# Kernel optimization log

Measured on AMD Instinct MI355X. Metric: run time of the kernel, lower is better.

The kernel has to match this reference:

```python
import jax, jax.numpy as jnp
import numpy as np

DIM = 256
HEADS = 8
SR = 2
EPS = 1e-5


def setup_inputs() -> dict:
    key = jax.random.key(0)
    ks = jax.random.split(key, 8)
    B, N, C = 4, 4096, DIM
    s = 0.02
    return {
        "x": jax.random.normal(ks[0], (B, N, C), dtype=jnp.float32),
        "H": 64,
        "W": 64,
        # sequence-reduction conv (Conv2d dim->dim, k=SR, stride=SR), OIHW
        "sr_w": jax.random.normal(ks[1], (C, C, SR, SR), dtype=jnp.float32) * s,
        "sr_b": jnp.zeros((C,), dtype=jnp.float32),
        "ln_g": jnp.ones((C,), dtype=jnp.float32),
        "ln_b": jnp.zeros((C,), dtype=jnp.float32),
        # torch Linear weights: y = x @ W.T (qkv_bias=False)
        "q_w": jax.random.normal(ks[2], (C, C), dtype=jnp.float32) * s,
        "kv_w": jax.random.normal(ks[3], (2 * C, C), dtype=jnp.float32) * s,
        "proj_w": jax.random.normal(ks[4], (C, C), dtype=jnp.float32) * s,
        "proj_b": jnp.zeros((C,), dtype=jnp.float32),
    }


def reference(x, H, W, sr_w, sr_b, ln_g, ln_b, q_w, kv_w, proj_w, proj_b):
    B, N, C = x.shape
    h, d = HEADS, C // HEADS
    scale = d ** -0.5

    # q: [B, h, N, d]
    q = (x @ q_w.T).reshape(B, N, h, d).transpose(0, 2, 1, 3)

    # sequence reduction: [B,N,C] -> [B,C,H,W] -> conv(k=SR, s=SR) -> [B, N', C]
    x_ = x.transpose(0, 2, 1).reshape(B, C, H, W)
    x_ = jax.lax.conv_general_dilated(
        x_, sr_w, window_strides=(SR, SR), padding="VALID",
        dimension_numbers=("NCHW", "OIHW", "NCHW"))
    x_ = x_ + sr_b[None, :, None, None]
    x_ = x_.reshape(B, C, -1).transpose(0, 2, 1)  # [B, N', C]

    # LayerNorm over C
    mu = x_.mean(-1, keepdims=True)
    var = x_.var(-1, keepdims=True)
    x_ = (x_ - mu) * jax.lax.rsqrt(var + EPS) * ln_g + ln_b

    # kv: [2, B, h, N', d]
    kv = (x_ @ kv_w.T).reshape(B, -1, 2, h, d).transpose(2, 0, 3, 1, 4)
    k, v = kv[0], kv[1]

    attn = jnp.einsum("bhnd,bhmd->bhnm", q, k) * scale
    attn = jax.nn.softmax(attn, axis=-1)  # attn_drop = 0 -> identity
    out = jnp.einsum("bhnm,bhmd->bhnd", attn, v)
    out = out.transpose(0, 2, 1, 3).reshape(B, N, C)

    return out @ proj_w.T + proj_b  # proj_drop = 0 -> identity
```

## Files before the change

### kernel.cpp

```cpp
#include <hip/hip_runtime.h>
#include <hip/hip_bf16.h>


typedef __attribute__((ext_vector_type(8))) short bf16x8;
typedef __attribute__((ext_vector_type(8))) unsigned short u16x8;
typedef __attribute__((ext_vector_type(4))) float f32x4;
typedef __attribute__((ext_vector_type(16))) float f32x16;
typedef __attribute__((ext_vector_type(2))) unsigned u32x2v;
typedef __attribute__((ext_vector_type(4))) unsigned u32x4v;

__device__ inline unsigned short f2bf(float f) {
  unsigned u = __float_as_uint(f);
  u += 0x7fffu + ((u >> 16) & 1u);
  return (unsigned short)(u >> 16);
}

__global__ __launch_bounds__(256) void prep_kernel(
    const float* __restrict__ x, unsigned short* __restrict__ x_bf,
    const float* __restrict__ srw, unsigned short* __restrict__ srw_bf) {
  const int bid = blockIdx.x, t = threadIdx.x;
  if (bid < 2048) {
    int i = bid * 256 + t;
    float4 a = reinterpret_cast<const float4*>(x)[i * 2];
    float4 b = reinterpret_cast<const float4*>(x)[i * 2 + 1];
    ushort4 lo, hi;
    lo.x = f2bf(a.x); lo.y = f2bf(a.y); lo.z = f2bf(a.z); lo.w = f2bf(a.w);
    hi.x = f2bf(b.x); hi.y = f2bf(b.y); hi.z = f2bf(b.z); hi.w = f2bf(b.w);
    reinterpret_cast<ushort4*>(x_bf)[i * 2] = lo;
    reinterpret_cast<ushort4*>(x_bf)[i * 2 + 1] = hi;
  } else {
    int o = bid - 2048;
    float4 v = reinterpret_cast<const float4*>(srw + (size_t)o * 1024)[t];
    srw_bf[(size_t)o * 1024 + 0 * 256 + t] = f2bf(v.x);
    srw_bf[(size_t)o * 1024 + 1 * 256 + t] = f2bf(v.y);
    srw_bf[(size_t)o * 1024 + 2 * 256 + t] = f2bf(v.z);
    srw_bf[(size_t)o * 1024 + 3 * 256 + t] = f2bf(v.w);
  }
}

__device__ __forceinline__ void gemm_body_q(
    const unsigned short* __restrict__ A, const float* __restrict__ W,
    unsigned short* __restrict__ C, int K, int N, float oscale,
    int m0, int n0, unsigned short* Asb, unsigned short* Bsb) {
  const int tid = threadIdx.x;
  const int w = tid >> 6, l = tid & 63, c = l & 15, g = l >> 4;
  const int wr = w >> 1, wc = w & 1;
  const int ar = tid >> 1, ah = tid & 1;
  const int bn = tid >> 2, bq = tid & 3;

  f32x4 acc[4][2];
#pragma unroll
  for (int mt = 0; mt < 4; ++mt)
#pragma unroll
    for (int nt = 0; nt < 2; ++nt)
#pragma unroll
      for (int r = 0; r < 4; ++r) acc[mt][nt][r] = 0.f;

  for (int k0 = 0; k0 < K; k0 += 32) {
    __syncthreads();
    {
      const unsigned short* asrc = A + (size_t)(m0 + ar) * K + k0 + ah * 16;
      u16x8 a0 = *reinterpret_cast<const u16x8*>(asrc);
      u16x8 a1 = *reinterpret_cast<const u16x8*>(asrc + 8);
      *reinterpret_cast<u16x8*>(&Asb[ar * 40 + ah * 16]) = a0;
      *reinterpret_cast<u16x8*>(&Asb[ar * 40 + ah * 16 + 8]) = a1;
    }
    {
      const float* wsrc = W + (size_t)(n0 + bn) * K + k0 + bq * 8;
      float4 w0 = *reinterpret_cast<const float4*>(wsrc);
      float4 w1 = *reinterpret_cast<const float4*>(wsrc + 4);
      u16x8 wb;
      wb[0] = f2bf(w0.x); wb[1] = f2bf(w0.y); wb[2] = f2bf(w0.z); wb[3] = f2bf(w0.w);
      wb[4] = f2bf(w1.x); wb[5] = f2bf(w1.y); wb[6] = f2bf(w1.z); wb[7] = f2bf(w1.w);
      *reinterpret_cast<u16x8*>(&Bsb[bn * 40 + bq * 8]) = wb;
    }
    __syncthreads();
    bf16x8 af[4], bfr[2];
#pragma unroll
    for (int mt = 0; mt < 4; ++mt)
      af[mt] = *reinterpret_cast<const bf16x8*>(
          &Asb[(wr * 64 + mt * 16 + c) * 40 + g * 8]);
#pragma unroll
    for (int nt = 0; nt < 2; ++nt)
      bfr[nt] = *reinterpret_cast<const bf16x8*>(
          &Bsb[(wc * 32 + nt * 16 + c) * 40 + g * 8]);
#pragma unroll
    for (int mt = 0; mt < 4; ++mt)
#pragma unroll
      for (int nt = 0; nt < 2; ++nt)
        acc[mt][nt] = __builtin_amdgcn_mfma_f32_16x16x32_bf16(
            af[mt], bfr[nt], acc[mt][nt], 0, 0, 0);
  }

#pragma unroll
  for (int mt = 0; mt < 4; ++mt)
#pragma unroll
    for (int nt = 0; nt < 2; ++nt) {
      int row = m0 + wr * 64 + mt * 16 + g * 4;
      int col = n0 + wc * 32 + nt * 16 + c;
#pragma unroll
      for (int r = 0; r < 4; ++r)
        C[(size_t)(row + r) * N + col] = f2bf(acc[mt][nt][r] * oscale);
    }
}

__device__ __forceinline__ void conv_body(
    const unsigned short* __restrict__ Xb, const unsigned short* __restrict__ Wp,
    const float* __restrict__ bias, float* __restrict__ C,
    int m0, int n0, unsigned short* Asb, unsigned short* Bsb) {
  const int tid = threadIdx.x;
  const int w = tid >> 6, l = tid & 63, c = l & 15, g = l >> 4;
  const int wr = w >> 1, wc = w & 1;
  const int sr = tid >> 2, sh = tid & 3;

  int base[4];
  {
    int row = m0 + sr;
    int b = row >> 10, o = row & 1023, oh = o >> 5, ow = o & 31;
#pragma unroll
    for (int tap = 0; tap < 4; ++tap) {
      int n = ((oh << 1) + (tap >> 1)) * 64 + (ow << 1) + (tap & 1);
      base[tap] = ((b << 12) + n) << 8;
    }
  }

  f32x4 acc[2][2];
#pragma unroll
  for (int mt = 0; mt < 2; ++mt)
#pragma unroll
    for (int nt = 0; nt < 2; ++nt)
#pragma unroll
      for (int r = 0; r < 4; ++r) acc[mt][nt][r] = 0.f;

  for (int k0 = 0; k0 < 1024; k0 += 32) {
    const int tap = k0 >> 8, ci0 = (k0 & 255) + sh * 8;
    __syncthreads();
    u16x8 av = *reinterpret_cast<const u16x8*>(&Xb[base[tap] + ci0]);
    *reinterpret_cast<u16x8*>(&Asb[sr * 40 + sh * 8]) = av;
    u16x8 wv = *reinterpret_cast<const u16x8*>(
        &Wp[(size_t)(n0 + sr) * 1024 + k0 + sh * 8]);
    *reinterpret_cast<u16x8*>(&Bsb[sr * 40 + sh * 8]) = wv;
    __syncthreads();
    bf16x8 af[2], bfr[2];
#pragma unroll
    for (int mt = 0; mt < 2; ++mt)
      af[mt] = *reinterpret_cast<const bf16x8*>(
          &Asb[(wr * 32 + mt * 16 + c) * 40 + g * 8]);
#pragma unroll
    for (int nt = 0; nt < 2; ++nt)
      bfr[nt] = *reinterpret_cast<const bf16x8*>(
          &Bsb[(wc * 32 + nt * 16 + c) * 40 + g * 8]);
#pragma unroll
    for (int mt = 0; mt < 2; ++mt)
#pragma unroll
      for (int nt = 0; nt < 2; ++nt)
        acc[mt][nt] = __builtin_amdgcn_mfma_f32_16x16x32_bf16(
            af[mt], bfr[nt], acc[mt][nt], 0, 0, 0);
  }

#pragma unroll
  for (int mt = 0; mt < 2; ++mt)
#pragma unroll
    for (int nt = 0; nt < 2; ++nt) {
      int row = m0 + wr * 32 + mt * 16 + g * 4;
      int col = n0 + wc * 32 + nt * 16 + c;
      float bv = bias[col];
#pragma unroll
      for (int r = 0; r < 4; ++r)
        C[(size_t)(row + r) * 256 + col] = acc[mt][nt][r] + bv;
    }
}

__global__ __launch_bounds__(256) void qconv_kernel(
    const unsigned short* __restrict__ x_bf, const float* __restrict__ q_w,
    unsigned short* __restrict__ q_bf, const unsigned short* __restrict__ srw_bf,
    const float* __restrict__ sr_b, float* __restrict__ xred, float qscale) {
  __shared__ unsigned short smem[128 * 40 + 64 * 40];
  const int bid = blockIdx.x;
  if (bid < 512) {
    gemm_body_q(x_bf, q_w, q_bf, 256, 256, qscale,
                (bid >> 2) * 128, (bid & 3) * 64, smem, smem + 128 * 40);
  } else {
    int cb = bid - 512;
    conv_body(x_bf, srw_bf, sr_b, xred,
              (cb >> 2) * 64, (cb & 3) * 64, smem, smem + 64 * 40);
  }
}

template <bool BF16_OUT, bool HAS_BIAS, bool KV_MODE>
__global__ __launch_bounds__(256) void mfma_gemm(
    const unsigned short* __restrict__ A, const float* __restrict__ W,
    const float* __restrict__ bias, void* __restrict__ Cv,
    void* __restrict__ Vtp, int M, int N, int K, float oscale) {
  __shared__ unsigned short Asb[128 * 40];
  __shared__ unsigned short Bsb[64 * 40];
  const int tid = threadIdx.x;
  const int w = tid >> 6, l = tid & 63, c = l & 15, g = l >> 4;
  const int wr = w >> 1, wc = w & 1;
  const int m0 = blockIdx.y * 128, n0 = blockIdx.x * 64;
  const int ar = tid >> 1, ah = tid & 1;
  const int bn = tid >> 2, bq = tid & 3;

  f32x4 acc[4][2];
#pragma unroll
  for (int mt = 0; mt < 4; ++mt)
#pragma unroll
    for (int nt = 0; nt < 2; ++nt)
#pragma unroll
      for (int r = 0; r < 4; ++r) acc[mt][nt][r] = 0.f;

  for (int k0 = 0; k0 < K; k0 += 32) {
    __syncthreads();
    {
      const unsigned short* asrc = A + (size_t)(m0 + ar) * K + k0 + ah * 16;
      u16x8 a0 = *reinterpret_cast<const u16x8*>(asrc);
      u16x8 a1 = *reinterpret_cast<const u16x8*>(asrc + 8);
      *reinterpret_cast<u16x8*>(&Asb[ar * 40 + ah * 16]) = a0;
      *reinterpret_cast<u16x8*>(&Asb[ar * 40 + ah * 16 + 8]) = a1;
    }
    {
      const float* wsrc = W + (size_t)(n0 + bn) * K + k0 + bq * 8;
      float4 w0 = *reinterpret_cast<const float4*>(wsrc);
      float4 w1 = *reinterpret_cast<const float4*>(wsrc + 4);
      u16x8 wb;
      wb[0] = f2bf(w0.x); wb[1] = f2bf(w0.y); wb[2] = f2bf(w0.z); wb[3] = f2bf(w0.w);
      wb[4] = f2bf(w1.x); wb[5] = f2bf(w1.y); wb[6] = f2bf(w1.z); wb[7] = f2bf(w1.w);
      *reinterpret_cast<u16x8*>(&Bsb[bn * 40 + bq * 8]) = wb;
    }
    __syncthreads();
    bf16x8 af[4], bfr[2];
#pragma unroll
    for (int mt = 0; mt < 4; ++mt)
      af[mt] = *reinterpret_cast<const bf16x8*>(
          &Asb[(wr * 64 + mt * 16 + c) * 40 + g * 8]);
#pragma unroll
    for (int nt = 0; nt < 2; ++nt)
      bfr[nt] = *reinterpret_cast<const bf16x8*>(
          &Bsb[(wc * 32 + nt * 16 + c) * 40 + g * 8]);
#pragma unroll
    for (int mt = 0; mt < 4; ++mt)
#pragma unroll
      for (int nt = 0; nt < 2; ++nt)
        acc[mt][nt] = __builtin_amdgcn_mfma_f32_16x16x32_bf16(
            af[mt], bfr[nt], acc[mt][nt], 0, 0, 0);
  }

#pragma unroll
  for (int mt = 0; mt < 4; ++mt)
#pragma unroll
    for (int nt = 0; nt < 2; ++nt) {
      int row = m0 + wr * 64 + mt * 16 + g * 4;
      int col = n0 + wc * 32 + nt * 16 + c;
      float bv = HAS_BIAS ? bias[col] : 0.f;
#pragma unroll
      for (int r = 0; r < 4; ++r) {
        float v = acc[mt][nt][r] * oscale + bv;
        if (KV_MODE) {
          if (col < 256) {
            ((unsigned short*)Cv)[(size_t)(row + r) * 256 + col] = f2bf(v);
          } else {
            int head = (col - 256) >> 5, d = (col - 256) & 31;
            int rr = row + r;
            ((unsigned short*)Vtp)[
                ((size_t)(((rr >> 10) << 3) + head) * 32 + d) * 1024 +
                (rr & 1023)] = f2bf(v);
          }
        } else if (BF16_OUT) {
          ((unsigned short*)Cv)[(size_t)(row + r) * N + col] = f2bf(v);
        } else {
          ((float*)Cv)[(size_t)(row + r) * N + col] = v;
        }
      }
    }
}

__global__ __launch_bounds__(256) void ln_kernel(
    const float* __restrict__ xr, const float* __restrict__ gam,
    const float* __restrict__ bet, unsigned short* __restrict__ xo) {
  const int row = blockIdx.x;
  const int t = threadIdx.x;
  float v = xr[(size_t)row * 256 + t];
  float s = v, s2 = v * v;
#pragma unroll
  for (int off = 32; off > 0; off >>= 1) {
    s  += __shfl_down(s, off, 64);
    s2 += __shfl_down(s2, off, 64);
  }
  __shared__ float red[8];
  const int wid = t >> 6;
  if ((t & 63) == 0) { red[wid] = s; red[wid + 4] = s2; }
  __syncthreads();
  s  = red[0] + red[1] + red[2] + red[3];
  s2 = red[4] + red[5] + red[6] + red[7];
  float mean = s * (1.f / 256.f);
  float var = s2 * (1.f / 256.f) - mean * mean;
  float rstd = rsqrtf(var + 1e-5f);
  xo[(size_t)row * 256 + t] = f2bf((v - mean) * rstd * gam[t] + bet[t]);
}

__global__ __launch_bounds__(128) void attn_mfma(
    const unsigned short* __restrict__ Qb,
    const unsigned short* __restrict__ Kb,
    const unsigned short* __restrict__ Vtg,
    unsigned short* __restrict__ O) {
  __shared__ __align__(16) unsigned short Vt[2][32][72];

  const int tid = threadIdx.x;
  const int l = tid & 63;
  const int w = tid >> 6;
  const int q32 = l & 31, hi = l >> 5;
  const int wg = blockIdx.x;
  const int qb = wg & 63, head = (wg >> 6) & 7, b = wg >> 9;
  const int hcol = head << 5;
  const int q0 = (b << 12) + (qb << 6) + (w << 5);

  bf16x8 qf[2];
  {
    const unsigned short* qp = Qb + (size_t)(q0 + q32) * 256 + hcol + hi * 8;
    qf[0] = *reinterpret_cast<const bf16x8*>(qp);
    qf[1] = *reinterpret_cast<const bf16x8*>(qp + 16);
  }

  const int sd = tid >> 2, skv = (tid & 3) << 4;
  const unsigned short* vtrow =
      Vtg + ((size_t)((b << 3) + head) * 32 + sd) * 1024 + skv;

  {
    u16x8 a = *reinterpret_cast<const u16x8*>(vtrow);
    u16x8 bv = *reinterpret_cast<const u16x8*>(vtrow + 8);
    *reinterpret_cast<u16x8*>(&Vt[0][sd][skv]) = a;
    *reinterpret_cast<u16x8*>(&Vt[0][sd][skv + 8]) = bv;
  }

  const unsigned short* kbase0 =
      Kb + ((size_t)(b << 10) + q32) * 256 + hcol + hi * 8;

  f32x16 acc;
#pragma unroll
  for (int r = 0; r < 16; ++r) acc[r] = 0.f;
  float lsum = 0.f;

  for (int t = 0; t < 16; ++t) {
    const int cur = t & 1;
    __syncthreads();

    u16x8 nv0, nv1;
    if (t < 15) {
      const unsigned short* vp = vtrow + (t + 1) * 64;
      nv0 = *reinterpret_cast<const u16x8*>(vp);
      nv1 = *reinterpret_cast<const u16x8*>(vp + 8);
    }

    const unsigned short* kbase = kbase0 + (size_t)t * 64 * 256;
    f32x16 s[2];
    {
      bf16x8 k00 = *reinterpret_cast<const bf16x8*>(kbase);
      bf16x8 k01 = *reinterpret_cast<const bf16x8*>(kbase + 16);
      bf16x8 k10 = *reinterpret_cast<const bf16x8*>(kbase + 32 * 256);
      bf16x8 k11 = *reinterpret_cast<const bf16x8*>(kbase + 32 * 256 + 16);
      f32x16 z;
#pragma unroll
      for (int r = 0; r < 16; ++r) z[r] = 0.f;
      s[0] = __builtin_amdgcn_mfma_f32_32x32x16_bf16(k00, qf[0], z, 0, 0, 0);
      s[0] = __builtin_amdgcn_mfma_f32_32x32x16_bf16(k01, qf[1], s[0], 0, 0, 0);
      s[1] = __builtin_amdgcn_mfma_f32_32x32x16_bf16(k10, qf[0], z, 0, 0, 0);
      s[1] = __builtin_amdgcn_mfma_f32_32x32x16_bf16(k11, qf[1], s[1], 0, 0, 0);
    }

#pragma unroll
    for (int kvb = 0; kvb < 2; ++kvb) {
      float p16[16];
#pragma unroll
      for (int r = 0; r < 16; ++r)
        p16[r] = __builtin_amdgcn_exp2f(s[kvb][r]);
      float s0 = (p16[0] + p16[1]) + (p16[2] + p16[3]);
      float s1 = (p16[4] + p16[5]) + (p16[6] + p16[7]);
      float s2 = (p16[8] + p16[9]) + (p16[10] + p16[11]);
      float s3 = (p16[12] + p16[13]) + (p16[14] + p16[15]);
      lsum += (s0 + s1) + (s2 + s3);
      unsigned A[8];
#pragma unroll
      for (int i = 0; i < 8; ++i) {
        unsigned o;
        asm("v_cvt_pk_bf16_f32 %0, %1, %2"
            : "=v"(o) : "v"(p16[2 * i]), "v"(p16[2 * i + 1]));
        A[i] = o;
      }
      u32x2v r02 = __builtin_amdgcn_permlane32_swap(A[0], A[2], false, false);
      u32x2v r13 = __builtin_amdgcn_permlane32_swap(A[1], A[3], false, false);
      u32x2v r46 = __builtin_amdgcn_permlane32_swap(A[4], A[6], false, false);
      u32x2v r57 = __builtin_amdgcn_permlane32_swap(A[5], A[7], false, false);
      u32x4v pk0 = {r02[0], r13[0], r02[1], r13[1]};
      u32x4v pk1 = {r46[0], r57[0], r46[1], r57[1]};
      bf16x8 pf0 = __builtin_bit_cast(bf16x8, pk0);
      bf16x8 pf1 = __builtin_bit_cast(bf16x8, pk1);
      const unsigned short* vrow = &Vt[cur][q32][kvb * 32 + hi * 8];
      bf16x8 vf0 = *reinterpret_cast<const bf16x8*>(vrow);
      bf16x8 vf1 = *reinterpret_cast<const bf16x8*>(vrow + 16);
      acc = __builtin_amdgcn_mfma_f32_32x32x16_bf16(vf0, pf0, acc, 0, 0, 0);
      acc = __builtin_amdgcn_mfma_f32_32x32x16_bf16(vf1, pf1, acc, 0, 0, 0);
    }

    if (t < 15) {
      *reinterpret_cast<u16x8*>(&Vt[cur ^ 1][sd][skv]) = nv0;
      *reinterpret_cast<u16x8*>(&Vt[cur ^ 1][sd][skv + 8]) = nv1;
    }
  }

  lsum += __shfl_xor(lsum, 32, 64);
  float inv = 1.f / lsum;
  unsigned short* orow = O + (size_t)(q0 + q32) * 256 + hcol;
#pragma unroll
  for (int rb = 0; rb < 4; ++rb) {
    const int d0 = rb * 8 + hi * 4;
    float a0 = acc[rb * 4 + 0] * inv, a1 = acc[rb * 4 + 1] * inv;
    float a2 = acc[rb * 4 + 2] * inv, a3 = acc[rb * 4 + 3] * inv;
    unsigned w0, w1;
    asm("v_cvt_pk_bf16_f32 %0, %1, %2" : "=v"(w0) : "v"(a0), "v"(a1));
    asm("v_cvt_pk_bf16_f32 %0, %1, %2" : "=v"(w1) : "v"(a2), "v"(a3));
    unsigned long long pk = (unsigned long long)w0 | ((unsigned long long)w1 << 32);
    *reinterpret_cast<unsigned long long*>(orow + d0) = pk;
  }
}

extern "C" void kernel_launch(void* const* d_in, const int* in_sizes, int n_in,
                              void* d_out, int out_size, void* d_ws,
                              size_t ws_size, hipStream_t stream) {
  const float* x      = (const float*)d_in[0];
  const float* sr_w   = (const float*)d_in[3];
  const float* sr_b   = (const float*)d_in[4];
  const float* ln_g   = (const float*)d_in[5];
  const float* ln_b   = (const float*)d_in[6];
  const float* q_w    = (const float*)d_in[7];
  const float* kv_w   = (const float*)d_in[8];
  const float* proj_w = (const float*)d_in[9];
  const float* proj_b = (const float*)d_in[10];
  float* out = (float*)d_out;

  char* ws = (char*)d_ws;
  unsigned short* x_bf    = (unsigned short*)(ws);
  unsigned short* q_bf    = (unsigned short*)(ws + 8388608);
  unsigned short* srw_bf  = (unsigned short*)(ws + 16777216);
  float*          xred    = (float*)(ws + 17301504);
  unsigned short* x_ln    = (unsigned short*)(ws + 21495808);
  unsigned short* k_buf   = (unsigned short*)(ws + 23592960);
  unsigned short* vt_buf  = (unsigned short*)(ws + 25690112);
  unsigned short* attn_bf = (unsigned short*)(ws + 27787264);

  const float qscale = 0.25506975154985854f;

  prep_kernel<<<2304, 256, 0, stream>>>(x, x_bf, sr_w, srw_bf);
  qconv_kernel<<<768, 256, 0, stream>>>(
      x_bf, q_w, q_bf, srw_bf, sr_b, xred, qscale);
  ln_kernel<<<4096, 256, 0, stream>>>(xred, ln_g, ln_b, x_ln);
  mfma_gemm<true, false, true><<<dim3(8, 32), 256, 0, stream>>>(
      x_ln, kv_w, nullptr, k_buf, vt_buf, 4096, 512, 256, 1.0f);
  attn_mfma<<<2048, 128, 0, stream>>>(q_bf, k_buf, vt_buf, attn_bf);
  mfma_gemm<false, true, false><<<dim3(4, 128), 256, 0, stream>>>(
      attn_bf, proj_w, proj_b, out, nullptr, 16384, 256, 256, 1.0f);
}
```

Baseline: 102.1 us.

## Fuse x bf16 conversion into GEMM/conv loads, stage K in LDS, vectorize LN

```diff
diff --git a/kernel.cpp b/kernel.cpp
--- a/kernel.cpp
+++ b/kernel.cpp
@@ -16,30 +16,17 @@
 }
 
 __global__ __launch_bounds__(256) void prep_kernel(
-    const float* __restrict__ x, unsigned short* __restrict__ x_bf,
     const float* __restrict__ srw, unsigned short* __restrict__ srw_bf) {
-  const int bid = blockIdx.x, t = threadIdx.x;
-  if (bid < 2048) {
-    int i = bid * 256 + t;
-    float4 a = reinterpret_cast<const float4*>(x)[i * 2];
-    float4 b = reinterpret_cast<const float4*>(x)[i * 2 + 1];
-    ushort4 lo, hi;
-    lo.x = f2bf(a.x); lo.y = f2bf(a.y); lo.z = f2bf(a.z); lo.w = f2bf(a.w);
-    hi.x = f2bf(b.x); hi.y = f2bf(b.y); hi.z = f2bf(b.z); hi.w = f2bf(b.w);
-    reinterpret_cast<ushort4*>(x_bf)[i * 2] = lo;
-    reinterpret_cast<ushort4*>(x_bf)[i * 2 + 1] = hi;
-  } else {
-    int o = bid - 2048;
-    float4 v = reinterpret_cast<const float4*>(srw + (size_t)o * 1024)[t];
-    srw_bf[(size_t)o * 1024 + 0 * 256 + t] = f2bf(v.x);
-    srw_bf[(size_t)o * 1024 + 1 * 256 + t] = f2bf(v.y);
-    srw_bf[(size_t)o * 1024 + 2 * 256 + t] = f2bf(v.z);
-    srw_bf[(size_t)o * 1024 + 3 * 256 + t] = f2bf(v.w);
-  }
+  const int o = blockIdx.x, t = threadIdx.x;
+  float4 v = reinterpret_cast<const float4*>(srw + (size_t)o * 1024)[t];
+  srw_bf[(size_t)o * 1024 + 0 * 256 + t] = f2bf(v.x);
+  srw_bf[(size_t)o * 1024 + 1 * 256 + t] = f2bf(v.y);
+  srw_bf[(size_t)o * 1024 + 2 * 256 + t] = f2bf(v.z);
+  srw_bf[(size_t)o * 1024 + 3 * 256 + t] = f2bf(v.w);
 }
 
 __device__ __forceinline__ void gemm_body_q(
-    const unsigned short* __restrict__ A, const float* __restrict__ W,
+    const float* __restrict__ Af, const float* __restrict__ W,
     unsigned short* __restrict__ C, int K, int N, float oscale,
     int m0, int n0, unsigned short* Asb, unsigned short* Bsb) {
   const int tid = threadIdx.x;
@@ -59,11 +46,18 @@
   for (int k0 = 0; k0 < K; k0 += 32) {
     __syncthreads();
     {
-      const unsigned short* asrc = A + (size_t)(m0 + ar) * K + k0 + ah * 16;
-      u16x8 a0 = *reinterpret_cast<const u16x8*>(asrc);
-      u16x8 a1 = *reinterpret_cast<const u16x8*>(asrc + 8);
-      *reinterpret_cast<u16x8*>(&Asb[ar * 40 + ah * 16]) = a0;
-      *reinterpret_cast<u16x8*>(&Asb[ar * 40 + ah * 16 + 8]) = a1;
+      const float* asrc = Af + (size_t)(m0 + ar) * K + k0 + ah * 16;
+      float4 a0 = *reinterpret_cast<const float4*>(asrc);
+      float4 a1 = *reinterpret_cast<const float4*>(asrc + 4);
+      float4 a2 = *reinterpret_cast<const float4*>(asrc + 8);
+      float4 a3 = *reinterpret_cast<const float4*>(asrc + 12);
+      u16x8 w0, w1;
+      w0[0] = f2bf(a0.x); w0[1] = f2bf(a0.y); w0[2] = f2bf(a0.z); w0[3] = f2bf(a0.w);
+      w0[4] = f2bf(a1.x); w0[5] = f2bf(a1.y); w0[6] = f2bf(a1.z); w0[7] = f2bf(a1.w);
+      w1[0] = f2bf(a2.x); w1[1] = f2bf(a2.y); w1[2] = f2bf(a2.z); w1[3] = f2bf(a2.w);
+      w1[4] = f2bf(a3.x); w1[5] = f2bf(a3.y); w1[6] = f2bf(a3.z); w1[7] = f2bf(a3.w);
+      *reinterpret_cast<u16x8*>(&Asb[ar * 40 + ah * 16]) = w0;
+      *reinterpret_cast<u16x8*>(&Asb[ar * 40 + ah * 16 + 8]) = w1;
     }
     {
       const float* wsrc = W + (size_t)(n0 + bn) * K + k0 + bq * 8;
@@ -105,7 +99,7 @@
 }
 
 __device__ __forceinline__ void conv_body(
-    const unsigned short* __restrict__ Xb, const unsigned short* __restrict__ Wp,
+    const float* __restrict__ Xf, const unsigned short* __restrict__ Wp,
     const float* __restrict__ bias, float* __restrict__ C,
     int m0, int n0, unsigned short* Asb, unsigned short* Bsb) {
   const int tid = threadIdx.x;
@@ -135,8 +129,15 @@
   for (int k0 = 0; k0 < 1024; k0 += 32) {
     const int tap = k0 >> 8, ci0 = (k0 & 255) + sh * 8;
     __syncthreads();
-    u16x8 av = *reinterpret_cast<const u16x8*>(&Xb[base[tap] + ci0]);
-    *reinterpret_cast<u16x8*>(&Asb[sr * 40 + sh * 8]) = av;
+    {
+      const float* xp = Xf + base[tap] + ci0;
+      float4 a0 = *reinterpret_cast<const float4*>(xp);
+      float4 a1 = *reinterpret_cast<const float4*>(xp + 4);
+      u16x8 av;
+      av[0] = f2bf(a0.x); av[1] = f2bf(a0.y); av[2] = f2bf(a0.z); av[3] = f2bf(a0.w);
+      av[4] = f2bf(a1.x); av[5] = f2bf(a1.y); av[6] = f2bf(a1.z); av[7] = f2bf(a1.w);
+      *reinterpret_cast<u16x8*>(&Asb[sr * 40 + sh * 8]) = av;
+    }
     u16x8 wv = *reinterpret_cast<const u16x8*>(
         &Wp[(size_t)(n0 + sr) * 1024 + k0 + sh * 8]);
     *reinterpret_cast<u16x8*>(&Bsb[sr * 40 + sh * 8]) = wv;
@@ -172,17 +173,17 @@
 }
 
 __global__ __launch_bounds__(256) void qconv_kernel(
-    const unsigned short* __restrict__ x_bf, const float* __restrict__ q_w,
+    const float* __restrict__ x, const float* __restrict__ q_w,
     unsigned short* __restrict__ q_bf, const unsigned short* __restrict__ srw_bf,
     const float* __restrict__ sr_b, float* __restrict__ xred, float qscale) {
   __shared__ unsigned short smem[128 * 40 + 64 * 40];
   const int bid = blockIdx.x;
   if (bid < 512) {
-    gemm_body_q(x_bf, q_w, q_bf, 256, 256, qscale,
+    gemm_body_q(x, q_w, q_bf, 256, 256, qscale,
                 (bid >> 2) * 128, (bid & 3) * 64, smem, smem + 128 * 40);
   } else {
     int cb = bid - 512;
-    conv_body(x_bf, srw_bf, sr_b, xred,
+    conv_body(x, srw_bf, sr_b, xred,
               (cb >> 2) * 64, (cb & 3) * 64, smem, smem + 64 * 40);
   }
 }
@@ -277,25 +278,29 @@
 __global__ __launch_bounds__(256) void ln_kernel(
     const float* __restrict__ xr, const float* __restrict__ gam,
     const float* __restrict__ bet, unsigned short* __restrict__ xo) {
-  const int row = blockIdx.x;
-  const int t = threadIdx.x;
-  float v = xr[(size_t)row * 256 + t];
-  float s = v, s2 = v * v;
+  const int w = threadIdx.x >> 6, l = threadIdx.x & 63;
+  const int row = blockIdx.x * 4 + w;
+  float4 v = *reinterpret_cast<const float4*>(xr + (size_t)row * 256 + l * 4);
+  float s = (v.x + v.y) + (v.z + v.w);
+  float s2 = (v.x * v.x + v.y * v.y) + (v.z * v.z + v.w * v.w);
 #pragma unroll
   for (int off = 32; off > 0; off >>= 1) {
-    s  += __shfl_down(s, off, 64);
-    s2 += __shfl_down(s2, off, 64);
-  }
-  __shared__ float red[8];
-  const int wid = t >> 6;
-  if ((t & 63) == 0) { red[wid] = s; red[wid + 4] = s2; }
-  __syncthreads();
-  s  = red[0] + red[1] + red[2] + red[3];
-  s2 = red[4] + red[5] + red[6] + red[7];
+    s  += __shfl_xor(s, off, 64);
+    s2 += __shfl_xor(s2, off, 64);
+  }
   float mean = s * (1.f / 256.f);
   float var = s2 * (1.f / 256.f) - mean * mean;
   float rstd = rsqrtf(var + 1e-5f);
-  xo[(size_t)row * 256 + t] = f2bf((v - mean) * rstd * gam[t] + bet[t]);
+  float4 g = *reinterpret_cast<const float4*>(gam + l * 4);
+  float4 bb = *reinterpret_cast<const float4*>(bet + l * 4);
+  unsigned short o0 = f2bf((v.x - mean) * rstd * g.x + bb.x);
+  unsigned short o1 = f2bf((v.y - mean) * rstd * g.y + bb.y);
+  unsigned short o2 = f2bf((v.z - mean) * rstd * g.z + bb.z);
+  unsigned short o3 = f2bf((v.w - mean) * rstd * g.w + bb.w);
+  unsigned long long pk =
+      (unsigned long long)o0 | ((unsigned long long)o1 << 16) |
+      ((unsigned long long)o2 << 32) | ((unsigned long long)o3 << 48);
+  *reinterpret_cast<unsigned long long*>(xo + (size_t)row * 256 + l * 4) = pk;
 }
 
 __global__ __launch_bounds__(128) void attn_mfma(
@@ -303,6 +308,7 @@
     const unsigned short* __restrict__ Kb,
     const unsigned short* __restrict__ Vtg,
     unsigned short* __restrict__ O) {
+  __shared__ __align__(16) unsigned short Kt[2][64][36];
   __shared__ __align__(16) unsigned short Vt[2][32][72];
 
   const int tid = threadIdx.x;
@@ -324,16 +330,20 @@
   const int sd = tid >> 2, skv = (tid & 3) << 4;
   const unsigned short* vtrow =
       Vtg + ((size_t)((b << 3) + head) * 32 + sd) * 1024 + skv;
+  const int kr = tid >> 1, kh = (tid & 1) << 4;
+  const unsigned short* ktrow =
+      Kb + ((size_t)(b << 10) + kr) * 256 + hcol + kh;
 
   {
-    u16x8 a = *reinterpret_cast<const u16x8*>(vtrow);
-    u16x8 bv = *reinterpret_cast<const u16x8*>(vtrow + 8);
-    *reinterpret_cast<u16x8*>(&Vt[0][sd][skv]) = a;
-    *reinterpret_cast<u16x8*>(&Vt[0][sd][skv + 8]) = bv;
-  }
-
-  const unsigned short* kbase0 =
-      Kb + ((size_t)(b << 10) + q32) * 256 + hcol + hi * 8;
+    u16x8 va = *reinterpret_cast<const u16x8*>(vtrow);
+    u16x8 vb = *reinterpret_cast<const u16x8*>(vtrow + 8);
+    *reinterpret_cast<u16x8*>(&Vt[0][sd][skv]) = va;
+    *reinterpret_cast<u16x8*>(&Vt[0][sd][skv + 8]) = vb;
+    u16x8 ka = *reinterpret_cast<const u16x8*>(ktrow);
+    u16x8 kb2 = *reinterpret_cast<const u16x8*>(ktrow + 8);
+    *reinterpret_cast<u16x8*>(&Kt[0][kr][kh]) = ka;
+    *reinterpret_cast<u16x8*>(&Kt[0][kr][kh + 8]) = kb2;
+  }
 
   f32x16 acc;
 #pragma unroll
@@ -344,20 +354,22 @@
     const int cur = t & 1;
     __syncthreads();
 
-    u16x8 nv0, nv1;
+    u16x8 nv0, nv1, nk0, nk1;
     if (t < 15) {
       const unsigned short* vp = vtrow + (t + 1) * 64;
       nv0 = *reinterpret_cast<const u16x8*>(vp);
       nv1 = *reinterpret_cast<const u16x8*>(vp + 8);
-    }
-
-    const unsigned short* kbase = kbase0 + (size_t)t * 64 * 256;
+      const unsigned short* kp = ktrow + (size_t)(t + 1) * 64 * 256;
+      nk0 = *reinterpret_cast<const u16x8*>(kp);
+      nk1 = *reinterpret_cast<const u16x8*>(kp + 8);
+    }
+
     f32x16 s[2];
     {
-      bf16x8 k00 = *reinterpret_cast<const bf16x8*>(kbase);
-      bf16x8 k01 = *reinterpret_cast<const bf16x8*>(kbase + 16);
-      bf16x8 k10 = *reinterpret_cast<const bf16x8*>(kbase + 32 * 256);
-      bf16x8 k11 = *reinterpret_cast<const bf16x8*>(kbase + 32 * 256 + 16);
+      bf16x8 k00 = *reinterpret_cast<const bf16x8*>(&Kt[cur][q32][hi * 8]);
+      bf16x8 k01 = *reinterpret_cast<const bf16x8*>(&Kt[cur][q32][hi * 8 + 16]);
+      bf16x8 k10 = *reinterpret_cast<const bf16x8*>(&Kt[cur][q32 + 32][hi * 8]);
+      bf16x8 k11 = *reinterpret_cast<const bf16x8*>(&Kt[cur][q32 + 32][hi * 8 + 16]);
       f32x16 z;
 #pragma unroll
       for (int r = 0; r < 16; ++r) z[r] = 0.f;
@@ -404,6 +416,8 @@
     if (t < 15) {
       *reinterpret_cast<u16x8*>(&Vt[cur ^ 1][sd][skv]) = nv0;
       *reinterpret_cast<u16x8*>(&Vt[cur ^ 1][sd][skv + 8]) = nv1;
+      *reinterpret_cast<u16x8*>(&Kt[cur ^ 1][kr][kh]) = nk0;
+      *reinterpret_cast<u16x8*>(&Kt[cur ^ 1][kr][kh + 8]) = nk1;
     }
   }
 
@@ -438,21 +452,20 @@
   float* out = (float*)d_out;
 
   char* ws = (char*)d_ws;
-  unsigned short* x_bf    = (unsigned short*)(ws);
-  unsigned short* q_bf    = (unsigned short*)(ws + 8388608);
-  unsigned short* srw_bf  = (unsigned short*)(ws + 16777216);
-  float*          xred    = (float*)(ws + 17301504);
-  unsigned short* x_ln    = (unsigned short*)(ws + 21495808);
-  unsigned short* k_buf   = (unsigned short*)(ws + 23592960);
-  unsigned short* vt_buf  = (unsigned short*)(ws + 25690112);
-  unsigned short* attn_bf = (unsigned short*)(ws + 27787264);
+  unsigned short* q_bf    = (unsigned short*)(ws);
+  unsigned short* srw_bf  = (unsigned short*)(ws + 8388608);
+  float*          xred    = (float*)(ws + 8912896);
+  unsigned short* x_ln    = (unsigned short*)(ws + 13107200);
+  unsigned short* k_buf   = (unsigned short*)(ws + 15204352);
+  unsigned short* vt_buf  = (unsigned short*)(ws + 17301504);
+  unsigned short* attn_bf = (unsigned short*)(ws + 19398656);
 
   const float qscale = 0.25506975154985854f;
 
-  prep_kernel<<<2304, 256, 0, stream>>>(x, x_bf, sr_w, srw_bf);
+  prep_kernel<<<256, 256, 0, stream>>>(sr_w, srw_bf);
   qconv_kernel<<<768, 256, 0, stream>>>(
-      x_bf, q_w, q_bf, srw_bf, sr_b, xred, qscale);
-  ln_kernel<<<4096, 256, 0, stream>>>(xred, ln_g, ln_b, x_ln);
+      x, q_w, q_bf, srw_bf, sr_b, xred, qscale);
+  ln_kernel<<<1024, 256, 0, stream>>>(xred, ln_g, ln_b, x_ln);
   mfma_gemm<true, false, true><<<dim3(8, 32), 256, 0, stream>>>(
       x_ln, kv_w, nullptr, k_buf, vt_buf, 4096, 512, 256, 1.0f);
   attn_mfma<<<2048, 128, 0, stream>>>(q_bf, k_buf, vt_buf, attn_bf);
```

After: 96.36 us. 5.7% less time.
